# Performance work log

Measured on AMD Instinct MI355X. Metric: run time of the kernel, lower is better.

The kernel has to match this reference:

```python
import jax, jax.numpy as jnp
import numpy as np
from jax import lax

N, P = 64, 7
C1, H1 = 256, 56
C2, H2 = 512, 28
C3, H3 = 1024, 14
HID1, HID2, HID3 = 256, 768, 1792
MLP1, MLP2, OUT = 3584, 1792, 512


def setup_inputs() -> dict:
    key = jax.random.key(0)
    ks = jax.random.split(key, 32)
    x1 = jax.random.normal(ks[0], (N, C1, H1, H1), jnp.float32)
    x2 = jax.random.normal(ks[1], (N, C2, H2, H2), jnp.float32)
    x3 = jax.random.normal(ks[2], (N, C3, H3, H3), jnp.float32)
    a = jax.random.randint(ks[3], (N, P, 2), 0, 56)
    b = jax.random.randint(ks[4], (N, P, 2), 0, 56)
    lo, hi = jnp.minimum(a, b), jnp.maximum(a, b)
    patchs = jnp.stack([lo[..., 0], hi[..., 0], lo[..., 1], hi[..., 1]], axis=-1)
    drop = jax.random.bernoulli(ks[5], 0.1, (N, P))
    patchs = jnp.where(drop[..., None], 0, patchs).astype(jnp.int32)

    def lin(k, o, i):
        return jax.random.normal(k, (o, i), jnp.float32) * 0.02

    def vec(k, o):
        return jax.random.normal(k, (o,), jnp.float32) * 0.02

    inp = {
        'x1': x1, 'x2': x2, 'x3': x3, 'patchs': patchs,
        # LSTM weights, torch gate order (i,f,g,o); bias = b_ih + b_hh combined
        'l1_wih': lin(ks[6], 4 * HID1, 256),  'l1_whh': lin(ks[7], 4 * HID1, HID1),  'l1_b': vec(ks[8], 4 * HID1),
        'l2_wih': lin(ks[9], 4 * HID2, 768),  'l2_whh': lin(ks[10], 4 * HID2, HID2), 'l2_b': vec(ks[11], 4 * HID2),
        'l3_wih': lin(ks[12], 4 * HID3, 1792),'l3_whh': lin(ks[13], 4 * HID3, HID3), 'l3_b': vec(ks[14], 4 * HID3),
        'aw1': lin(ks[15], MLP1, P * HID3), 'ab1': vec(ks[16], MLP1),
        'aw2': lin(ks[17], MLP2, MLP1),     'ab2': vec(ks[18], MLP2),
        'aw3': lin(ks[19], P, MLP2),        'ab3': vec(ks[20], P),
        'fw':  lin(ks[21], OUT, HID3),      'fb':  vec(ks[22], OUT),
    }
    return inp


def _crop_avg(x, patchs, num, den):
    """Batched data-dependent crop + avg-pool via 2D integral image.
    x: [N,C,H,W]; patchs: [N,P,4] ints (y0,y1,x0,x1) at 56-scale. Returns [N,P,C]."""
    y0 = (patchs[..., 0] * num) // den
    y1 = (patchs[..., 1] * num) // den
    x0 = (patchs[..., 2] * num) // den
    x1 = (patchs[..., 3] * num) // den
    S = jnp.cumsum(jnp.cumsum(x, axis=2), axis=3)
    S = jnp.pad(S, ((0, 0), (0, 0), (1, 0), (1, 0)))  # [N,C,H+1,W+1]
    bidx = jnp.arange(x.shape[0])[:, None]

    def g(Y, X):
        return S[bidx, :, Y, X]  # advanced idx split by ':' -> [N,P,C]

    tot = g(y1 + 1, x1 + 1) - g(y0, x1 + 1) - g(y1 + 1, x0) + g(y0, x0)
    area = ((y1 - y0 + 1) * (x1 - x0 + 1)).astype(x.dtype)[..., None]
    avg = tot / area
    zero = jnp.all(patchs == 0, axis=-1)  # all-zero box -> zero feature
    return jnp.where(zero[..., None], jnp.zeros((), x.dtype), avg)


def _lstm(x, wih, whh, b):
    """Single-layer batch-first LSTM, torch gate order i,f,g,o. x: [N,T,D] -> [N,T,H]."""
    Nb, T, _ = x.shape
    H = whh.shape[1]
    xg = jnp.einsum('ntd,gd->ntg', x, wih) + b  # precompute input gates

    def step(carry, xt):
        h, c = carry
        gates = xt + h @ whh.T
        i, f, g, o = jnp.split(gates, 4, axis=-1)
        c = jax.nn.sigmoid(f) * c + jax.nn.sigmoid(i) * jnp.tanh(g)
        h = jax.nn.sigmoid(o) * jnp.tanh(c)
        return (h, c), h

    h0 = jnp.zeros((Nb, H), x.dtype)
    _, hs = lax.scan(step, (h0, h0), jnp.swapaxes(xg, 0, 1))
    return jnp.swapaxes(hs, 0, 1)


def reference(x1, x2, x3, patchs,
              l1_wih, l1_whh, l1_b, l2_wih, l2_whh, l2_b, l3_wih, l3_whh, l3_b,
              aw1, ab1, aw2, ab2, aw3, ab3, fw, fb):
    local1 = _crop_avg(x1, patchs, 55, 55)                     # [N,7,256]
    rnn1 = _lstm(local1, l1_wih, l1_whh, l1_b)                 # [N,7,256]
    local2 = jnp.concatenate([_crop_avg(x2, patchs, 27, 55), rnn1], axis=2)   # [N,7,768]
    rnn2 = _lstm(local2, l2_wih, l2_whh, l2_b)                 # [N,7,768]
    local3 = jnp.concatenate([_crop_avg(x3, patchs, 13, 55), rnn2], axis=2)   # [N,7,1792]
    rnn3 = _lstm(local3, l3_wih, l3_whh, l3_b)                 # [N,7,1792]
    # attention pooling (dropout = identity in eval)
    flat = rnn3.reshape(rnn3.shape[0], -1)                     # [N,7*1792]
    h = jax.nn.relu(flat @ aw1.T + ab1)
    h = jax.nn.relu(h @ aw2.T + ab2)
    attn = jax.nn.relu(h @ aw3.T + ab3)                        # [N,7]
    alpha = jax.nn.softmax(attn, axis=1)
    feat = jnp.sum(rnn3 * alpha[:, :, None], axis=1)           # [N,1792]
    return feat @ fw.T + fb                                    # [N,512]
```

## Files before the change

kernel.cpp:

```cpp
#include <hip/hip_runtime.h>
#include <hip/hip_bf16.h>
#include <math.h>

#define NB 64
#define PP 7

typedef __attribute__((ext_vector_type(8))) short short8;
typedef __attribute__((ext_vector_type(4))) float f32x4;

static __device__ inline unsigned bf16r(float f) {
    unsigned u = __builtin_bit_cast(unsigned, f);
    u += 0x7fffu + ((u >> 16) & 1u);
    return u >> 16;
}
static __device__ inline unsigned pack2(float a, float b) {
    return bf16r(a) | (bf16r(b) << 16);
}

template<int H, int VEC, int GRP>
__global__ __launch_bounds__(256) void crop_kernel(
    const float* __restrict__ x, const int* __restrict__ patchs,
    float* __restrict__ out, int C, int num, int den, int ldo, int col0)
{
    constexpr int USED = H / VEC;
    constexpr int PPWAVE = 64 / GRP;
    int tid = threadIdx.x, lane = tid & 63, wv = tid >> 6;
    int n = blockIdx.y;
    int sub = lane / GRP, xl = lane & (GRP - 1);
    bool act = xl < USED;
    int c = blockIdx.x * (4 * PPWAVE) + wv * PPWAVE + sub;

    int y0m1[PP], y1s[PP], x0s[PP], x1s[PP], zer[PP];
    float rarea[PP];
    #pragma unroll
    for (int p = 0; p < PP; ++p) {
        int p0 = patchs[(n * PP + p) * 4 + 0];
        int p1 = patchs[(n * PP + p) * 4 + 1];
        int p2 = patchs[(n * PP + p) * 4 + 2];
        int p3 = patchs[(n * PP + p) * 4 + 3];
        int y0 = p0 * num / den, y1 = p1 * num / den;
        int xx0 = p2 * num / den, xx1 = p3 * num / den;
        y0m1[p] = y0 - 1; y1s[p] = y1; x0s[p] = xx0; x1s[p] = xx1;
        rarea[p] = 1.f / (float)((y1 - y0 + 1) * (xx1 - xx0 + 1));
        zer[p] = (p0 | p1 | p2 | p3) == 0;
    }

    const float* pl = x + ((size_t)n * C + c) * (H * H) + (act ? xl * VEC : 0);

    float cc[VEC];
    float lo[PP][VEC], hi[PP][VEC];
    #pragma unroll
    for (int e = 0; e < VEC; ++e) cc[e] = 0.f;
    #pragma unroll
    for (int p = 0; p < PP; ++p)
        #pragma unroll
        for (int e = 0; e < VEC; ++e) { lo[p][e] = 0.f; hi[p][e] = 0.f; }

    #pragma unroll 4
    for (int y = 0; y < H; ++y) {
        float v[VEC];
        if constexpr (VEC == 4) {
            float4 t = *reinterpret_cast<const float4*>(pl + y * H);
            v[0] = t.x; v[1] = t.y; v[2] = t.z; v[3] = t.w;
        } else {
            float2 t = *reinterpret_cast<const float2*>(pl + y * H);
            v[0] = t.x; v[1] = t.y;
        }
        #pragma unroll
        for (int e = 0; e < VEC; ++e) cc[e] += v[e];
        #pragma unroll
        for (int p = 0; p < PP; ++p) {
            #pragma unroll
            for (int e = 0; e < VEC; ++e) {
                lo[p][e] = (y == y0m1[p]) ? cc[e] : lo[p][e];
                hi[p][e] = (y == y1s[p]) ? cc[e] : hi[p][e];
            }
        }
    }

    #pragma unroll
    for (int p = 0; p < PP; ++p) {
        float d = 0.f;
        #pragma unroll
        for (int e = 0; e < VEC; ++e) {
            int col = xl * VEC + e;
            if (col >= x0s[p] && col <= x1s[p]) d += hi[p][e] - lo[p][e];
        }
        #pragma unroll
        for (int off = GRP / 2; off >= 1; off >>= 1)
            d += __shfl_xor(d, off, 64);
        if (act && xl == 0)
            out[(size_t)(n * PP + p) * ldo + col0 + c] = zer[p] ? 0.f : d * rarea[p];
    }
}

__global__ __launch_bounds__(256) void gemm64_kernel(
    const float* __restrict__ X, int ldx,
    const float* __restrict__ W, int K,
    const float* __restrict__ bias,
    float* __restrict__ out, int ldo,
    int kchunk, int partial)
{
    __shared__ short Xs[64][72];
    __shared__ short Ws[64][72];
    int tid = threadIdx.x;
    int lane = tid & 63, wv = tid >> 6;
    int m0 = blockIdx.y * 64;
    int o0 = blockIdx.x * 64;
    int z = blockIdx.z;
    int kbeg = z * kchunk, kend = kbeg + kchunk;

    f32x4 acc[4];
    #pragma unroll
    for (int i = 0; i < 4; ++i) acc[i] = (f32x4){0.f, 0.f, 0.f, 0.f};

    for (int kb = kbeg; kb < kend; kb += 64) {
        #pragma unroll
        for (int i = 0; i < 2; ++i) {
            int cch = tid + 256 * i;
            int r = cch >> 3, col = (cch & 7) * 8;
            const float* src = X + (size_t)(m0 + r) * ldx + kb + col;
            float4 a = *reinterpret_cast<const float4*>(src);
            float4 b = *reinterpret_cast<const float4*>(src + 4);
            uint4 v;
            v.x = pack2(a.x, a.y); v.y = pack2(a.z, a.w);
            v.z = pack2(b.x, b.y); v.w = pack2(b.z, b.w);
            *reinterpret_cast<uint4*>(&Xs[r][col]) = v;
            const float* srcw = W + (size_t)(o0 + r) * K + kb + col;
            float4 c = *reinterpret_cast<const float4*>(srcw);
            float4 d = *reinterpret_cast<const float4*>(srcw + 4);
            uint4 w;
            w.x = pack2(c.x, c.y); w.y = pack2(c.z, c.w);
            w.z = pack2(d.x, d.y); w.w = pack2(d.z, d.w);
            *reinterpret_cast<uint4*>(&Ws[r][col]) = w;
        }
        __syncthreads();
        #pragma unroll
        for (int kk = 0; kk < 64; kk += 32) {
            int ro = lane & 15, kof = kk + (lane >> 4) * 8;
            short8 b = *reinterpret_cast<const short8*>(&Ws[wv * 16 + ro][kof]);
            #pragma unroll
            for (int i = 0; i < 4; ++i) {
                short8 a = *reinterpret_cast<const short8*>(&Xs[16 * i + ro][kof]);
                acc[i] = __builtin_amdgcn_mfma_f32_16x16x32_bf16(a, b, acc[i], 0, 0, 0);
            }
        }
        __syncthreads();
    }

    float* dst = out;
    if (partial) dst += (size_t)z * (gridDim.y * 64) * ldo;
    int o = o0 + wv * 16 + (lane & 15);
    float bv = (!partial && bias) ? bias[o] : 0.f;
    int mr = (lane >> 4) * 4;
    #pragma unroll
    for (int i = 0; i < 4; ++i) {
        #pragma unroll
        for (int r = 0; r < 4; ++r) {
            int m = m0 + 16 * i + mr + r;
            dst[(size_t)m * ldo + o] = acc[i][r] + bv;
        }
    }
}

__global__ __launch_bounds__(256) void reduce_kernel(
    const float* __restrict__ partial, int S, int M, int O,
    const float* __restrict__ bias, int relu, float* __restrict__ out)
{
    int idx = blockIdx.x * 256 + threadIdx.x;
    int tot = M * O;
    if (idx >= tot) return;
    float v = bias[idx % O];
    for (int s = 0; s < S; ++s) v += partial[(size_t)s * tot + idx];
    if (relu) v = fmaxf(v, 0.f);
    out[idx] = v;
}

__global__ __launch_bounds__(256) void lstm_cell_kernel(
    const float* __restrict__ partial, int S,
    const float* __restrict__ xgt, int ldxg,
    float* __restrict__ h, float* __restrict__ c,
    float* __restrict__ dest, int Hd, int ldd, int first)
{
    int idx = blockIdx.x * 256 + threadIdx.x;
    int q = Hd >> 2;
    if (idx >= NB * q) return;
    int n = idx / q, j4 = (idx - n * q) * 4;
    int H4 = 4 * Hd;

    f32x4 g[4];
    #pragma unroll
    for (int gi = 0; gi < 4; ++gi)
        g[gi] = *reinterpret_cast<const f32x4*>(xgt + (size_t)n * ldxg + gi * Hd + j4);
    if (!first) {
        for (int s = 0; s < S; ++s) {
            const float* pr = partial + ((size_t)s * NB + n) * H4;
            #pragma unroll
            for (int gi = 0; gi < 4; ++gi)
                g[gi] += *reinterpret_cast<const f32x4*>(pr + gi * Hd + j4);
        }
    }
    f32x4 cp = (f32x4){0.f, 0.f, 0.f, 0.f};
    if (!first) cp = *reinterpret_cast<const f32x4*>(c + (size_t)n * Hd + j4);

    f32x4 cn, hn;
    #pragma unroll
    for (int k = 0; k < 4; ++k) {
        float si = 1.f / (1.f + expf(-g[0][k]));
        float sf = 1.f / (1.f + expf(-g[1][k]));
        float so = 1.f / (1.f + expf(-g[3][k]));
        float cc = sf * cp[k] + si * tanhf(g[2][k]);
        cn[k] = cc;
        hn[k] = so * tanhf(cc);
    }
    *reinterpret_cast<f32x4*>(c + (size_t)n * Hd + j4) = cn;
    *reinterpret_cast<f32x4*>(h + (size_t)n * Hd + j4) = hn;
    *reinterpret_cast<f32x4*>(dest + (size_t)n * ldd + j4) = hn;
}

__global__ __launch_bounds__(256) void aw3_kernel(
    const float* __restrict__ h2, const float* __restrict__ aw3,
    const float* __restrict__ ab3, float* __restrict__ attnb)
{
    int n = blockIdx.x;
    int lane = threadIdx.x & 63, wv = threadIdx.x >> 6;
    for (int p = wv; p < PP; p += 4) {
        float s = 0.f;
        for (int k = lane; k < 1792; k += 64)
            s += h2[n * 1792 + k] * aw3[p * 1792 + k];
        #pragma unroll
        for (int off = 32; off; off >>= 1) s += __shfl_down(s, off, 64);
        if (lane == 0) attnb[n * PP + p] = fmaxf(s + ab3[p], 0.f);
    }
}

__global__ __launch_bounds__(256) void attn_pool_kernel(
    const float* __restrict__ attn, const float* __restrict__ rnn3,
    float* __restrict__ feat)
{
    int n = blockIdx.x;
    __shared__ float alpha[PP];
    if (threadIdx.x == 0) {
        float a[PP], mx = -1e30f;
        for (int p = 0; p < PP; ++p) { a[p] = attn[n * PP + p]; mx = fmaxf(mx, a[p]); }
        float s = 0.f;
        for (int p = 0; p < PP; ++p) { a[p] = expf(a[p] - mx); s += a[p]; }
        for (int p = 0; p < PP; ++p) alpha[p] = a[p] / s;
    }
    __syncthreads();
    for (int j = threadIdx.x; j < 1792; j += 256) {
        float s = 0.f;
        #pragma unroll
        for (int p = 0; p < PP; ++p)
            s += rnn3[((size_t)n * PP + p) * 1792 + j] * alpha[p];
        feat[(size_t)n * 1792 + j] = s;
    }
}


extern "C" void kernel_launch(void* const* d_in, const int* in_sizes, int n_in,
                              void* d_out, int out_size, void* d_ws, size_t ws_size,
                              hipStream_t stream) {
    const float* x1 = (const float*)d_in[0];
    const float* x2 = (const float*)d_in[1];
    const float* x3 = (const float*)d_in[2];
    const int* patchs = (const int*)d_in[3];
    const float* l1_wih = (const float*)d_in[4];
    const float* l1_whh = (const float*)d_in[5];
    const float* l1_b   = (const float*)d_in[6];
    const float* l2_wih = (const float*)d_in[7];
    const float* l2_whh = (const float*)d_in[8];
    const float* l2_b   = (const float*)d_in[9];
    const float* l3_wih = (const float*)d_in[10];
    const float* l3_whh = (const float*)d_in[11];
    const float* l3_b   = (const float*)d_in[12];
    const float* aw1 = (const float*)d_in[13];
    const float* ab1 = (const float*)d_in[14];
    const float* aw2 = (const float*)d_in[15];
    const float* ab2 = (const float*)d_in[16];
    const float* aw3 = (const float*)d_in[17];
    const float* ab3 = (const float*)d_in[18];
    const float* fw  = (const float*)d_in[19];
    const float* fb  = (const float*)d_in[20];
    float* out = (float*)d_out;

    float* ws = (float*)d_ws;
    float* local1 = ws;
    float* local2 = local1 + 114688;
    float* local3 = local2 + 344064;
    float* rnn3   = local3;
    float* xg     = local3 + 802816;
    float* partial= xg + 3211264;
    float* hbuf   = partial + 1835008;
    float* cbuf   = hbuf + 114688;
    float* h1     = cbuf + 114688;
    float* h2     = h1 + 229376;
    float* attnb  = h2 + 114688;
    float* feat   = attnb + 512;

    crop_kernel<56, 4, 16><<<dim3(16, NB), 256, 0, stream>>>(
        x1, patchs, local1, 256, 55, 55, 256, 0);
    crop_kernel<28, 4, 8><<<dim3(16, NB), 256, 0, stream>>>(
        x2, patchs, local2, 512, 27, 55, 768, 0);
    crop_kernel<14, 2, 8><<<dim3(32, NB), 256, 0, stream>>>(
        x3, patchs, local3, 1024, 13, 55, 1792, 0);

    struct LstmCfg {
        const float *Xbuf, *wih, *whh, *b;
        int D, H, recS, reckchunk;
        float* dest_base; int destHT, col0;
    };
    LstmCfg cfgs[3] = {
        { local1, l1_wih, l1_whh, l1_b, 256, 256, 4, 64, local2, 768, 512 },
        { local2, l2_wih, l2_whh, l2_b, 768, 768, 6, 128, local3, 1792, 1024 },
        { local3, l3_wih, l3_whh, l3_b, 1792, 1792, 4, 448, rnn3, 1792, 0 },
    };
    for (int L = 0; L < 3; ++L) {
        LstmCfg& cf = cfgs[L];
        int H4 = 4 * cf.H;
        int cellblk = (NB * cf.H / 4 + 255) / 256;
        gemm64_kernel<<<dim3(H4 / 64, 7, 1), 256, 0, stream>>>(
            cf.Xbuf, cf.D, cf.wih, cf.D, cf.b, xg, H4, cf.D, 0);
        for (int t = 0; t < PP; ++t) {
            if (t > 0) {
                gemm64_kernel<<<dim3(H4 / 64, 1, cf.recS), 256, 0, stream>>>(
                    hbuf, cf.H, cf.whh, cf.H, nullptr, partial, H4, cf.reckchunk, 1);
            }
            float* dest = cf.dest_base + (size_t)t * cf.destHT + cf.col0;
            lstm_cell_kernel<<<cellblk, 256, 0, stream>>>(
                partial, cf.recS, xg + (size_t)t * H4, PP * H4,
                hbuf, cbuf, dest, cf.H, PP * cf.destHT, t == 0);
        }
    }

    gemm64_kernel<<<dim3(56, 1, 7), 256, 0, stream>>>(
        rnn3, 12544, aw1, 12544, nullptr, partial, 3584, 1792, 1);
    reduce_kernel<<<(64 * 3584 + 255) / 256, 256, 0, stream>>>(
        partial, 7, 64, 3584, ab1, 1, h1);
    gemm64_kernel<<<dim3(28, 1, 4), 256, 0, stream>>>(
        h1, 3584, aw2, 3584, nullptr, partial, 1792, 896, 1);
    reduce_kernel<<<(64 * 1792 + 255) / 256, 256, 0, stream>>>(
        partial, 4, 64, 1792, ab2, 1, h2);
    aw3_kernel<<<NB, 256, 0, stream>>>(h2, aw3, ab3, attnb);
    attn_pool_kernel<<<NB, 256, 0, stream>>>(attnb, rnn3, feat);
    gemm64_kernel<<<dim3(8, 1, 7), 256, 0, stream>>>(
        feat, 1792, fw, 1792, nullptr, partial, 512, 256, 1);
    reduce_kernel<<<(64 * 512 + 255) / 256, 256, 0, stream>>>(
        partial, 7, 64, 512, fb, 0, out);
}
```

Baseline: 641.2 us.

## Fuse LSTM recurrent GEMM with cell update and merge attention kernels

Replaces the per-timestep split-K recurrent GEMM plus separate cell kernel with one kernel per step. Each block computes a 16-unit slice of all four gates for all 64 batch rows with bf16 MFMA, then applies the cell update in-register via shared memory. The h buffer is double-buffered so blocks can read the previous h while writing the new one. The attention logit and pooling kernels are also merged into one. This removes launches and the partial-sum round trip through global memory. The cost is fewer blocks per step (H/16, as few as 16 for layer 1) with no K-split, so each block walks the full K dimension serially.

```diff
diff --git a/kernel.cpp b/kernel.cpp
--- a/kernel.cpp
+++ b/kernel.cpp
@@ -163,6 +163,89 @@
     }
 }
 
+__global__ __launch_bounds__(256) void lstm_step_kernel(
+    const float* __restrict__ hprev, const float* __restrict__ whh,
+    const float* __restrict__ xgt, int ldxg,
+    float* __restrict__ hnew, float* __restrict__ c,
+    float* __restrict__ dest, int ldd, int H, int first)
+{
+    __shared__ short Hs[64][72];
+    __shared__ short Ws[64][72];
+    __shared__ float gbuf[4][64][20];
+    int tid = threadIdx.x, lane = tid & 63, wv = tid >> 6;
+    int j0 = blockIdx.x * 16;
+
+    if (!first) {
+        f32x4 acc[4];
+        #pragma unroll
+        for (int i = 0; i < 4; ++i) acc[i] = (f32x4){0.f, 0.f, 0.f, 0.f};
+        for (int kb = 0; kb < H; kb += 64) {
+            #pragma unroll
+            for (int i = 0; i < 2; ++i) {
+                int cch = tid + 256 * i;
+                int r = cch >> 3, col = (cch & 7) * 8;
+                const float* src = hprev + (size_t)r * H + kb + col;
+                float4 a = *reinterpret_cast<const float4*>(src);
+                float4 bb = *reinterpret_cast<const float4*>(src + 4);
+                uint4 v;
+                v.x = pack2(a.x, a.y); v.y = pack2(a.z, a.w);
+                v.z = pack2(bb.x, bb.y); v.w = pack2(bb.z, bb.w);
+                *reinterpret_cast<uint4*>(&Hs[r][col]) = v;
+                int wr = (r >> 4) * H + j0 + (r & 15);
+                const float* srcw = whh + (size_t)wr * H + kb + col;
+                float4 cc = *reinterpret_cast<const float4*>(srcw);
+                float4 dd = *reinterpret_cast<const float4*>(srcw + 4);
+                uint4 w;
+                w.x = pack2(cc.x, cc.y); w.y = pack2(cc.z, cc.w);
+                w.z = pack2(dd.x, dd.y); w.w = pack2(dd.z, dd.w);
+                *reinterpret_cast<uint4*>(&Ws[r][col]) = w;
+            }
+            __syncthreads();
+            #pragma unroll
+            for (int kk = 0; kk < 64; kk += 32) {
+                int ro = lane & 15, kof = kk + (lane >> 4) * 8;
+                short8 b = *reinterpret_cast<const short8*>(&Ws[wv * 16 + ro][kof]);
+                #pragma unroll
+                for (int i = 0; i < 4; ++i) {
+                    short8 a = *reinterpret_cast<const short8*>(&Hs[16 * i + ro][kof]);
+                    acc[i] = __builtin_amdgcn_mfma_f32_16x16x32_bf16(a, b, acc[i], 0, 0, 0);
+                }
+            }
+            __syncthreads();
+        }
+        int mr = (lane >> 4) * 4, jj = lane & 15;
+        #pragma unroll
+        for (int i = 0; i < 4; ++i)
+            #pragma unroll
+            for (int r = 0; r < 4; ++r)
+                gbuf[wv][16 * i + mr + r][jj] = acc[i][r];
+        __syncthreads();
+    }
+
+    int n = tid >> 2, jq = (tid & 3) * 4;
+    f32x4 g[4];
+    #pragma unroll
+    for (int gi = 0; gi < 4; ++gi) {
+        g[gi] = *reinterpret_cast<const f32x4*>(&xgt[(size_t)n * ldxg + gi * H + j0 + jq]);
+        if (!first) g[gi] += *reinterpret_cast<const f32x4*>(&gbuf[gi][n][jq]);
+    }
+    f32x4 cp = (f32x4){0.f, 0.f, 0.f, 0.f};
+    if (!first) cp = *reinterpret_cast<const f32x4*>(&c[(size_t)n * H + j0 + jq]);
+    f32x4 cn, hn;
+    #pragma unroll
+    for (int k = 0; k < 4; ++k) {
+        float si = 1.f / (1.f + expf(-g[0][k]));
+        float sf = 1.f / (1.f + expf(-g[1][k]));
+        float so = 1.f / (1.f + expf(-g[3][k]));
+        float ccv = sf * cp[k] + si * tanhf(g[2][k]);
+        cn[k] = ccv;
+        hn[k] = so * tanhf(ccv);
+    }
+    *reinterpret_cast<f32x4*>(&c[(size_t)n * H + j0 + jq]) = cn;
+    *reinterpret_cast<f32x4*>(&hnew[(size_t)n * H + j0 + jq]) = hn;
+    *reinterpret_cast<f32x4*>(&dest[(size_t)n * ldd + j0 + jq]) = hn;
+}
+
 __global__ __launch_bounds__(256) void reduce_kernel(
     const float* __restrict__ partial, int S, int M, int O,
     const float* __restrict__ bias, int relu, float* __restrict__ out)
@@ -176,79 +259,33 @@
     out[idx] = v;
 }
 
-__global__ __launch_bounds__(256) void lstm_cell_kernel(
-    const float* __restrict__ partial, int S,
-    const float* __restrict__ xgt, int ldxg,
-    float* __restrict__ h, float* __restrict__ c,
-    float* __restrict__ dest, int Hd, int ldd, int first)
-{
-    int idx = blockIdx.x * 256 + threadIdx.x;
-    int q = Hd >> 2;
-    if (idx >= NB * q) return;
-    int n = idx / q, j4 = (idx - n * q) * 4;
-    int H4 = 4 * Hd;
-
-    f32x4 g[4];
-    #pragma unroll
-    for (int gi = 0; gi < 4; ++gi)
-        g[gi] = *reinterpret_cast<const f32x4*>(xgt + (size_t)n * ldxg + gi * Hd + j4);
-    if (!first) {
-        for (int s = 0; s < S; ++s) {
-            const float* pr = partial + ((size_t)s * NB + n) * H4;
-            #pragma unroll
-            for (int gi = 0; gi < 4; ++gi)
-                g[gi] += *reinterpret_cast<const f32x4*>(pr + gi * Hd + j4);
-        }
-    }
-    f32x4 cp = (f32x4){0.f, 0.f, 0.f, 0.f};
-    if (!first) cp = *reinterpret_cast<const f32x4*>(c + (size_t)n * Hd + j4);
-
-    f32x4 cn, hn;
-    #pragma unroll
-    for (int k = 0; k < 4; ++k) {
-        float si = 1.f / (1.f + expf(-g[0][k]));
-        float sf = 1.f / (1.f + expf(-g[1][k]));
-        float so = 1.f / (1.f + expf(-g[3][k]));
-        float cc = sf * cp[k] + si * tanhf(g[2][k]);
-        cn[k] = cc;
-        hn[k] = so * tanhf(cc);
-    }
-    *reinterpret_cast<f32x4*>(c + (size_t)n * Hd + j4) = cn;
-    *reinterpret_cast<f32x4*>(h + (size_t)n * Hd + j4) = hn;
-    *reinterpret_cast<f32x4*>(dest + (size_t)n * ldd + j4) = hn;
-}
-
-__global__ __launch_bounds__(256) void aw3_kernel(
+__global__ __launch_bounds__(256) void attn_fused_kernel(
     const float* __restrict__ h2, const float* __restrict__ aw3,
-    const float* __restrict__ ab3, float* __restrict__ attnb)
+    const float* __restrict__ ab3, const float* __restrict__ rnn3,
+    float* __restrict__ feat)
 {
     int n = blockIdx.x;
-    int lane = threadIdx.x & 63, wv = threadIdx.x >> 6;
+    int tid = threadIdx.x, lane = tid & 63, wv = tid >> 6;
+    __shared__ float logit[PP];
+    __shared__ float alpha[PP];
     for (int p = wv; p < PP; p += 4) {
         float s = 0.f;
         for (int k = lane; k < 1792; k += 64)
             s += h2[n * 1792 + k] * aw3[p * 1792 + k];
         #pragma unroll
         for (int off = 32; off; off >>= 1) s += __shfl_down(s, off, 64);
-        if (lane == 0) attnb[n * PP + p] = fmaxf(s + ab3[p], 0.f);
-    }
-}
-
-__global__ __launch_bounds__(256) void attn_pool_kernel(
-    const float* __restrict__ attn, const float* __restrict__ rnn3,
-    float* __restrict__ feat)
-{
-    int n = blockIdx.x;
-    __shared__ float alpha[PP];
-    if (threadIdx.x == 0) {
+        if (lane == 0) logit[p] = fmaxf(s + ab3[p], 0.f);
+    }
+    __syncthreads();
+    if (tid == 0) {
         float a[PP], mx = -1e30f;
-        for (int p = 0; p < PP; ++p) { a[p] = attn[n * PP + p]; mx = fmaxf(mx, a[p]); }
+        for (int p = 0; p < PP; ++p) { a[p] = logit[p]; mx = fmaxf(mx, a[p]); }
         float s = 0.f;
         for (int p = 0; p < PP; ++p) { a[p] = expf(a[p] - mx); s += a[p]; }
         for (int p = 0; p < PP; ++p) alpha[p] = a[p] / s;
     }
     __syncthreads();
-    for (int j = threadIdx.x; j < 1792; j += 256) {
+    for (int j = tid; j < 1792; j += 256) {
         float s = 0.f;
         #pragma unroll
         for (int p = 0; p < PP; ++p)
@@ -291,12 +328,12 @@
     float* rnn3   = local3;
     float* xg     = local3 + 802816;
     float* partial= xg + 3211264;
-    float* hbuf   = partial + 1835008;
-    float* cbuf   = hbuf + 114688;
+    float* hbufA  = partial + 1835008;
+    float* hbufB  = hbufA + 114688;
+    float* cbuf   = hbufB + 114688;
     float* h1     = cbuf + 114688;
     float* h2     = h1 + 229376;
-    float* attnb  = h2 + 114688;
-    float* feat   = attnb + 512;
+    float* feat   = h2 + 114688;
 
     crop_kernel<56, 4, 16><<<dim3(16, NB), 256, 0, stream>>>(
         x1, patchs, local1, 256, 55, 55, 256, 0);
@@ -307,29 +344,26 @@
 
     struct LstmCfg {
         const float *Xbuf, *wih, *whh, *b;
-        int D, H, recS, reckchunk;
+        int D, H;
         float* dest_base; int destHT, col0;
     };
     LstmCfg cfgs[3] = {
-        { local1, l1_wih, l1_whh, l1_b, 256, 256, 4, 64, local2, 768, 512 },
-        { local2, l2_wih, l2_whh, l2_b, 768, 768, 6, 128, local3, 1792, 1024 },
-        { local3, l3_wih, l3_whh, l3_b, 1792, 1792, 4, 448, rnn3, 1792, 0 },
+        { local1, l1_wih, l1_whh, l1_b, 256, 256, local2, 768, 512 },
+        { local2, l2_wih, l2_whh, l2_b, 768, 768, local3, 1792, 1024 },
+        { local3, l3_wih, l3_whh, l3_b, 1792, 1792, rnn3, 1792, 0 },
     };
     for (int L = 0; L < 3; ++L) {
         LstmCfg& cf = cfgs[L];
         int H4 = 4 * cf.H;
-        int cellblk = (NB * cf.H / 4 + 255) / 256;
         gemm64_kernel<<<dim3(H4 / 64, 7, 1), 256, 0, stream>>>(
             cf.Xbuf, cf.D, cf.wih, cf.D, cf.b, xg, H4, cf.D, 0);
         for (int t = 0; t < PP; ++t) {
-            if (t > 0) {
-                gemm64_kernel<<<dim3(H4 / 64, 1, cf.recS), 256, 0, stream>>>(
-                    hbuf, cf.H, cf.whh, cf.H, nullptr, partial, H4, cf.reckchunk, 1);
-            }
+            float* hp = (t & 1) ? hbufB : hbufA;
+            float* hw = (t & 1) ? hbufA : hbufB;
             float* dest = cf.dest_base + (size_t)t * cf.destHT + cf.col0;
-            lstm_cell_kernel<<<cellblk, 256, 0, stream>>>(
-                partial, cf.recS, xg + (size_t)t * H4, PP * H4,
-                hbuf, cbuf, dest, cf.H, PP * cf.destHT, t == 0);
+            lstm_step_kernel<<<cf.H / 16, 256, 0, stream>>>(
+                hp, cf.whh, xg + (size_t)t * H4, PP * H4,
+                hw, cbuf, dest, PP * cf.destHT, cf.H, t == 0);
         }
     }
 
@@ -341,8 +375,7 @@
         h1, 3584, aw2, 3584, nullptr, partial, 1792, 896, 1);
     reduce_kernel<<<(64 * 1792 + 255) / 256, 256, 0, stream>>>(
         partial, 4, 64, 1792, ab2, 1, h2);
-    aw3_kernel<<<NB, 256, 0, stream>>>(h2, aw3, ab3, attnb);
-    attn_pool_kernel<<<NB, 256, 0, stream>>>(attnb, rnn3, feat);
+    attn_fused_kernel<<<NB, 256, 0, stream>>>(h2, aw3, ab3, rnn3, feat);
     gemm64_kernel<<<dim3(8, 1, 7), 256, 0, stream>>>(
         feat, 1792, fw, 1792, nullptr, partial, 512, 256, 1);
     reduce_kernel<<<(64 * 512 + 255) / 256, 256, 0, stream>>>(
```

New measurement: 731.2 us. 14.1% more time.

## Pre-convert LSTM weights to bf16, widen GEMM N-tile, fuse attention kernels

Applied to the files above, without the earlier changes.

Recurrent and layer-3 input weights are converted to bf16 once per call in a new conversion kernel. The recurrent GEMMs then load 16-byte bf16 rows instead of converting fp32 on every timestep. The GEMM is templated on N-tile width (256 for layer 3 and aw1) so each X tile feeds more MFMAs and the X tile is reloaded fewer times. The aw3 logits and softmax pooling kernels are merged into one. The conversion pass adds extra traffic and launches each call, which pays off only through the repeated recurrent-weight reads, and the wider tiles cut block counts for layer 3.

```diff
diff --git a/kernel.cpp b/kernel.cpp
--- a/kernel.cpp
+++ b/kernel.cpp
@@ -15,6 +15,19 @@
 }
 static __device__ inline unsigned pack2(float a, float b) {
     return bf16r(a) | (bf16r(b) << 16);
+}
+
+__global__ __launch_bounds__(256) void cvt_kernel(
+    const float* __restrict__ in, uint4* __restrict__ out, int n8)
+{
+    int idx = blockIdx.x * 256 + threadIdx.x;
+    if (idx >= n8) return;
+    const float4* p = reinterpret_cast<const float4*>(in) + 2 * (size_t)idx;
+    float4 a = p[0], b = p[1];
+    uint4 v;
+    v.x = pack2(a.x, a.y); v.y = pack2(a.z, a.w);
+    v.z = pack2(b.x, b.y); v.w = pack2(b.z, b.w);
+    out[idx] = v;
 }
 
 template<int H, int VEC, int GRP>
@@ -94,25 +107,30 @@
     }
 }
 
-__global__ __launch_bounds__(256) void gemm64_kernel(
+template<int BN, bool WBF>
+__global__ __launch_bounds__(256) void gemm_kernel(
     const float* __restrict__ X, int ldx,
-    const float* __restrict__ W, int K,
+    const void* __restrict__ Wp, int K,
     const float* __restrict__ bias,
     float* __restrict__ out, int ldo,
     int kchunk, int partial)
 {
+    constexpr int NF = BN / 64;
     __shared__ short Xs[64][72];
-    __shared__ short Ws[64][72];
+    __shared__ short Ws[BN][72];
     int tid = threadIdx.x;
     int lane = tid & 63, wv = tid >> 6;
     int m0 = blockIdx.y * 64;
-    int o0 = blockIdx.x * 64;
+    int o0 = blockIdx.x * BN;
     int z = blockIdx.z;
     int kbeg = z * kchunk, kend = kbeg + kchunk;
 
-    f32x4 acc[4];
-    #pragma unroll
-    for (int i = 0; i < 4; ++i) acc[i] = (f32x4){0.f, 0.f, 0.f, 0.f};
+    f32x4 acc[4][NF];
+    #pragma unroll
+    for (int i = 0; i < 4; ++i)
+        #pragma unroll
+        for (int j = 0; j < NF; ++j)
+            acc[i][j] = (f32x4){0.f, 0.f, 0.f, 0.f};
 
     for (int kb = kbeg; kb < kend; kb += 64) {
         #pragma unroll
@@ -126,23 +144,41 @@
             v.x = pack2(a.x, a.y); v.y = pack2(a.z, a.w);
             v.z = pack2(b.x, b.y); v.w = pack2(b.z, b.w);
             *reinterpret_cast<uint4*>(&Xs[r][col]) = v;
-            const float* srcw = W + (size_t)(o0 + r) * K + kb + col;
-            float4 c = *reinterpret_cast<const float4*>(srcw);
-            float4 d = *reinterpret_cast<const float4*>(srcw + 4);
-            uint4 w;
-            w.x = pack2(c.x, c.y); w.y = pack2(c.z, c.w);
-            w.z = pack2(d.x, d.y); w.w = pack2(d.z, d.w);
-            *reinterpret_cast<uint4*>(&Ws[r][col]) = w;
+        }
+        #pragma unroll
+        for (int i = 0; i < 2 * NF; ++i) {
+            int cch = tid + 256 * i;
+            int r = cch >> 3, col = (cch & 7) * 8;
+            if constexpr (WBF) {
+                const short* srcw = (const short*)Wp + (size_t)(o0 + r) * K + kb + col;
+                *reinterpret_cast<uint4*>(&Ws[r][col]) =
+                    *reinterpret_cast<const uint4*>(srcw);
+            } else {
+                const float* srcw = (const float*)Wp + (size_t)(o0 + r) * K + kb + col;
+                float4 c = *reinterpret_cast<const float4*>(srcw);
+                float4 d = *reinterpret_cast<const float4*>(srcw + 4);
+                uint4 w;
+                w.x = pack2(c.x, c.y); w.y = pack2(c.z, c.w);
+                w.z = pack2(d.x, d.y); w.w = pack2(d.z, d.w);
+                *reinterpret_cast<uint4*>(&Ws[r][col]) = w;
+            }
         }
         __syncthreads();
         #pragma unroll
         for (int kk = 0; kk < 64; kk += 32) {
             int ro = lane & 15, kof = kk + (lane >> 4) * 8;
-            short8 b = *reinterpret_cast<const short8*>(&Ws[wv * 16 + ro][kof]);
+            short8 b[NF];
+            #pragma unroll
+            for (int j = 0; j < NF; ++j)
+                b[j] = *reinterpret_cast<const short8*>(
+                    &Ws[wv * (BN / 4) + 16 * j + ro][kof]);
             #pragma unroll
             for (int i = 0; i < 4; ++i) {
                 short8 a = *reinterpret_cast<const short8*>(&Xs[16 * i + ro][kof]);
-                acc[i] = __builtin_amdgcn_mfma_f32_16x16x32_bf16(a, b, acc[i], 0, 0, 0);
+                #pragma unroll
+                for (int j = 0; j < NF; ++j)
+                    acc[i][j] = __builtin_amdgcn_mfma_f32_16x16x32_bf16(
+                        a, b[j], acc[i][j], 0, 0, 0);
             }
         }
         __syncthreads();
@@ -150,15 +186,18 @@
 
     float* dst = out;
     if (partial) dst += (size_t)z * (gridDim.y * 64) * ldo;
-    int o = o0 + wv * 16 + (lane & 15);
-    float bv = (!partial && bias) ? bias[o] : 0.f;
     int mr = (lane >> 4) * 4;
     #pragma unroll
-    for (int i = 0; i < 4; ++i) {
-        #pragma unroll
-        for (int r = 0; r < 4; ++r) {
-            int m = m0 + 16 * i + mr + r;
-            dst[(size_t)m * ldo + o] = acc[i][r] + bv;
+    for (int j = 0; j < NF; ++j) {
+        int o = o0 + wv * (BN / 4) + 16 * j + (lane & 15);
+        float bv = (!partial && bias) ? bias[o] : 0.f;
+        #pragma unroll
+        for (int i = 0; i < 4; ++i) {
+            #pragma unroll
+            for (int r = 0; r < 4; ++r) {
+                int m = m0 + 16 * i + mr + r;
+                dst[(size_t)m * ldo + o] = acc[i][j][r] + bv;
+            }
         }
     }
 }
@@ -218,37 +257,33 @@
     *reinterpret_cast<f32x4*>(dest + (size_t)n * ldd + j4) = hn;
 }
 
-__global__ __launch_bounds__(256) void aw3_kernel(
+__global__ __launch_bounds__(256) void attn_fused_kernel(
     const float* __restrict__ h2, const float* __restrict__ aw3,
-    const float* __restrict__ ab3, float* __restrict__ attnb)
+    const float* __restrict__ ab3, const float* __restrict__ rnn3,
+    float* __restrict__ feat)
 {
     int n = blockIdx.x;
-    int lane = threadIdx.x & 63, wv = threadIdx.x >> 6;
+    int tid = threadIdx.x, lane = tid & 63, wv = tid >> 6;
+    __shared__ float logit[PP];
+    __shared__ float alpha[PP];
     for (int p = wv; p < PP; p += 4) {
         float s = 0.f;
         for (int k = lane; k < 1792; k += 64)
             s += h2[n * 1792 + k] * aw3[p * 1792 + k];
         #pragma unroll
         for (int off = 32; off; off >>= 1) s += __shfl_down(s, off, 64);
-        if (lane == 0) attnb[n * PP + p] = fmaxf(s + ab3[p], 0.f);
-    }
-}
-
-__global__ __launch_bounds__(256) void attn_pool_kernel(
-    const float* __restrict__ attn, const float* __restrict__ rnn3,
-    float* __restrict__ feat)
-{
-    int n = blockIdx.x;
-    __shared__ float alpha[PP];
-    if (threadIdx.x == 0) {
+        if (lane == 0) logit[p] = fmaxf(s + ab3[p], 0.f);
+    }
+    __syncthreads();
+    if (tid == 0) {
         float a[PP], mx = -1e30f;
-        for (int p = 0; p < PP; ++p) { a[p] = attn[n * PP + p]; mx = fmaxf(mx, a[p]); }
+        for (int p = 0; p < PP; ++p) { a[p] = logit[p]; mx = fmaxf(mx, a[p]); }
         float s = 0.f;
         for (int p = 0; p < PP; ++p) { a[p] = expf(a[p] - mx); s += a[p]; }
         for (int p = 0; p < PP; ++p) alpha[p] = a[p] / s;
     }
     __syncthreads();
-    for (int j = threadIdx.x; j < 1792; j += 256) {
+    for (int j = tid; j < 1792; j += 256) {
         float s = 0.f;
         #pragma unroll
         for (int p = 0; p < PP; ++p)
@@ -291,12 +326,25 @@
     float* rnn3   = local3;
     float* xg     = local3 + 802816;
     float* partial= xg + 3211264;
-    float* hbuf   = partial + 1835008;
+    float* hbuf   = partial + 3211264;
     float* cbuf   = hbuf + 114688;
     float* h1     = cbuf + 114688;
     float* h2     = h1 + 229376;
-    float* attnb  = h2 + 114688;
-    float* feat   = attnb + 512;
+    float* feat   = h2 + 114688;
+    float* wb     = feat + 114688;
+    short* whh1b  = (short*)wb;
+    short* whh2b  = (short*)(wb + 131072);
+    short* whh3b  = (short*)(wb + 131072 + 1179648);
+    short* wih3b  = (short*)(wb + 131072 + 1179648 + 6422528);
+
+    cvt_kernel<<<(262144 / 8 + 255) / 256, 256, 0, stream>>>(
+        l1_whh, (uint4*)whh1b, 262144 / 8);
+    cvt_kernel<<<(2359296 / 8 + 255) / 256, 256, 0, stream>>>(
+        l2_whh, (uint4*)whh2b, 2359296 / 8);
+    cvt_kernel<<<(12845056 / 8 + 255) / 256, 256, 0, stream>>>(
+        l3_whh, (uint4*)whh3b, 12845056 / 8);
+    cvt_kernel<<<(12845056 / 8 + 255) / 256, 256, 0, stream>>>(
+        l3_wih, (uint4*)wih3b, 12845056 / 8);
 
     crop_kernel<56, 4, 16><<<dim3(16, NB), 256, 0, stream>>>(
         x1, patchs, local1, 256, 55, 55, 256, 0);
@@ -305,45 +353,56 @@
     crop_kernel<14, 2, 8><<<dim3(32, NB), 256, 0, stream>>>(
         x3, patchs, local3, 1024, 13, 55, 1792, 0);
 
-    struct LstmCfg {
-        const float *Xbuf, *wih, *whh, *b;
-        int D, H, recS, reckchunk;
-        float* dest_base; int destHT, col0;
-    };
-    LstmCfg cfgs[3] = {
-        { local1, l1_wih, l1_whh, l1_b, 256, 256, 4, 64, local2, 768, 512 },
-        { local2, l2_wih, l2_whh, l2_b, 768, 768, 6, 128, local3, 1792, 1024 },
-        { local3, l3_wih, l3_whh, l3_b, 1792, 1792, 4, 448, rnn3, 1792, 0 },
-    };
-    for (int L = 0; L < 3; ++L) {
-        LstmCfg& cf = cfgs[L];
-        int H4 = 4 * cf.H;
-        int cellblk = (NB * cf.H / 4 + 255) / 256;
-        gemm64_kernel<<<dim3(H4 / 64, 7, 1), 256, 0, stream>>>(
-            cf.Xbuf, cf.D, cf.wih, cf.D, cf.b, xg, H4, cf.D, 0);
+    {
+        int H = 256, H4 = 1024;
+        gemm_kernel<64, false><<<dim3(16, 7, 1), 256, 0, stream>>>(
+            local1, 256, l1_wih, 256, l1_b, xg, H4, 256, 0);
         for (int t = 0; t < PP; ++t) {
-            if (t > 0) {
-                gemm64_kernel<<<dim3(H4 / 64, 1, cf.recS), 256, 0, stream>>>(
-                    hbuf, cf.H, cf.whh, cf.H, nullptr, partial, H4, cf.reckchunk, 1);
-            }
-            float* dest = cf.dest_base + (size_t)t * cf.destHT + cf.col0;
-            lstm_cell_kernel<<<cellblk, 256, 0, stream>>>(
-                partial, cf.recS, xg + (size_t)t * H4, PP * H4,
-                hbuf, cbuf, dest, cf.H, PP * cf.destHT, t == 0);
-        }
-    }
-
-    gemm64_kernel<<<dim3(56, 1, 7), 256, 0, stream>>>(
+            if (t > 0)
+                gemm_kernel<64, true><<<dim3(16, 1, 4), 256, 0, stream>>>(
+                    hbuf, H, whh1b, H, nullptr, partial, H4, 64, 1);
+            lstm_cell_kernel<<<(NB * H / 4 + 255) / 256, 256, 0, stream>>>(
+                partial, 4, xg + (size_t)t * H4, PP * H4,
+                hbuf, cbuf, local2 + (size_t)t * 768 + 512, H, PP * 768, t == 0);
+        }
+    }
+    {
+        int H = 768, H4 = 3072;
+        gemm_kernel<64, false><<<dim3(48, 7, 1), 256, 0, stream>>>(
+            local2, 768, l2_wih, 768, l2_b, xg, H4, 768, 0);
+        for (int t = 0; t < PP; ++t) {
+            if (t > 0)
+                gemm_kernel<64, true><<<dim3(48, 1, 6), 256, 0, stream>>>(
+                    hbuf, H, whh2b, H, nullptr, partial, H4, 128, 1);
+            lstm_cell_kernel<<<(NB * H / 4 + 255) / 256, 256, 0, stream>>>(
+                partial, 6, xg + (size_t)t * H4, PP * H4,
+                hbuf, cbuf, local3 + (size_t)t * 1792 + 1024, H, PP * 1792, t == 0);
+        }
+    }
+    {
+        int H = 1792, H4 = 7168;
+        gemm_kernel<256, true><<<dim3(28, 7, 1), 256, 0, stream>>>(
+            local3, 1792, wih3b, 1792, l3_b, xg, H4, 1792, 0);
+        for (int t = 0; t < PP; ++t) {
+            if (t > 0)
+                gemm_kernel<256, true><<<dim3(28, 1, 7), 256, 0, stream>>>(
+                    hbuf, H, whh3b, H, nullptr, partial, H4, 256, 1);
+            lstm_cell_kernel<<<(NB * H / 4 + 255) / 256, 256, 0, stream>>>(
+                partial, 7, xg + (size_t)t * H4, PP * H4,
+                hbuf, cbuf, rnn3 + (size_t)t * 1792, H, PP * 1792, t == 0);
+        }
+    }
+
+    gemm_kernel<256, false><<<dim3(14, 1, 7), 256, 0, stream>>>(
         rnn3, 12544, aw1, 12544, nullptr, partial, 3584, 1792, 1);
     reduce_kernel<<<(64 * 3584 + 255) / 256, 256, 0, stream>>>(
         partial, 7, 64, 3584, ab1, 1, h1);
-    gemm64_kernel<<<dim3(28, 1, 4), 256, 0, stream>>>(
+    gemm_kernel<64, false><<<dim3(28, 1, 4), 256, 0, stream>>>(
         h1, 3584, aw2, 3584, nullptr, partial, 1792, 896, 1);
     reduce_kernel<<<(64 * 1792 + 255) / 256, 256, 0, stream>>>(
         partial, 4, 64, 1792, ab2, 1, h2);
-    aw3_kernel<<<NB, 256, 0, stream>>>(h2, aw3, ab3, attnb);
-    attn_pool_kernel<<<NB, 256, 0, stream>>>(attnb, rnn3, feat);
-    gemm64_kernel<<<dim3(8, 1, 7), 256, 0, stream>>>(
+    attn_fused_kernel<<<NB, 256, 0, stream>>>(h2, aw3, ab3, rnn3, feat);
+    gemm_kernel<64, false><<<dim3(8, 1, 7), 256, 0, stream>>>(
         feat, 1792, fw, 1792, nullptr, partial, 512, 256, 1);
     reduce_kernel<<<(64 * 512 + 255) / 256, 256, 0, stream>>>(
         partial, 7, 64, 512, fb, 0, out);
```

Result: slower. 736.2 us (+14.8%).
